# Kernel tuning notes

Hardware: AMD Instinct MI355X
Metric: run time of the kernel (lower is better)

## Reference

```python
import jax, jax.numpy as jnp
import numpy as np

B, C, H, W = 8, 128, 64, 64
GROUPS = 8
EPS = 1e-5


def setup_inputs() -> dict:
    key = jax.random.key(0)
    ks = jax.random.split(key, 4)
    x = jax.random.normal(ks[0], (B, C, H, W), dtype=jnp.float32)
    gamma = jnp.ones((C,), jnp.float32)
    beta = jnp.zeros((C,), jnp.float32)
    w_qkv = jax.random.normal(ks[1], (3 * C, C), jnp.float32) * (C ** -0.5)
    b_qkv = jnp.zeros((3 * C,), jnp.float32)
    w_proj = jax.random.normal(ks[2], (C, C), jnp.float32) * (C ** -0.5)
    b_proj = jnp.zeros((C,), jnp.float32)
    return {"x": x, "gamma": gamma, "beta": beta, "w_qkv": w_qkv,
            "b_qkv": b_qkv, "w_proj": w_proj, "b_proj": b_proj}


def group_norm(x, gamma, beta):
    b, c, h, w = x.shape
    xg = x.reshape(b, GROUPS, c // GROUPS, h, w)
    mean = xg.mean(axis=(2, 3, 4), keepdims=True)
    var = xg.var(axis=(2, 3, 4), keepdims=True)
    xn = ((xg - mean) * jax.lax.rsqrt(var + EPS)).reshape(b, c, h, w)
    return xn * gamma[None, :, None, None] + beta[None, :, None, None]


def reference(x, gamma, beta, w_qkv, b_qkv, w_proj, b_proj):
    b, c, h, w = x.shape
    n = h * w
    hn = group_norm(x, gamma, beta)
    # 1x1 conv == channel matmul
    qkv = jnp.einsum('oc,bchw->bohw', w_qkv, hn) + b_qkv[None, :, None, None]
    q, k, v = jnp.split(qkv.reshape(b, 3 * c, n), 3, axis=1)  # each [b,c,n]
    attn = jax.nn.softmax(jnp.einsum('bci,bcj->bij', q, k) * (c ** -0.5), axis=-1)
    out = jnp.einsum('bij,bcj->bci', attn, v).reshape(b, c, h, w)
    proj = jnp.einsum('oc,bchw->bohw', w_proj, out) + b_proj[None, :, None, None]
    return x + proj
```

## Files before the change

kernel.cpp:

```cpp
#include <hip/hip_runtime.h>
#include <cstdint>

#define NB 8
#define NC 128
#define NPIX 4096
#define NGROUP 8
#define CPG 16
#define EPS_GN 1e-5f
#define QSCALE 0.12751879523604132f
#define NSPLIT 2
#define JTILES (NPIX / 64 / NSPLIT)

typedef __attribute__((ext_vector_type(8))) short short8;
typedef __attribute__((ext_vector_type(16))) float f32x16;
typedef __attribute__((ext_vector_type(2))) int int2v;

typedef __attribute__((address_space(1))) const void gvoid_t;
typedef __attribute__((address_space(3))) void svoid_t;

__device__ __forceinline__ unsigned packbf(float lo, float hi) {
  unsigned r;
  asm("v_cvt_pk_bf16_f32 %0, %1, %2" : "=v"(r) : "v"(lo), "v"(hi));
  return r;
}
__device__ __forceinline__ ushort bf16of(float v) {
  return (ushort)(packbf(v, v) & 0xffffu);
}
__device__ __forceinline__ float bfl(unsigned w) {
  return __builtin_bit_cast(float, w << 16);
}
__device__ __forceinline__ float bfh(unsigned w) {
  return __builtin_bit_cast(float, w & 0xffff0000u);
}

__device__ __forceinline__ void plswap(unsigned& a, unsigned& b) {
  int2v r = __builtin_amdgcn_permlane32_swap((int)a, (int)b, false, false);
  a = (unsigned)r[0];
  b = (unsigned)r[1];
}

__device__ __forceinline__ int swK(int row) {
  return ((row & 7) << 1) | ((row >> 3) & 1);
}

__global__ __launch_bounds__(256) void k_pre(const float* __restrict__ x,
                                             float* __restrict__ stats,
                                             const float* __restrict__ wqkv,
                                             const float* __restrict__ wproj,
                                             ushort* __restrict__ wbuf) {
  int blk = blockIdx.x;
  if (blk < 64) {
    const float4* base = (const float4*)(x + (size_t)blk * CPG * NPIX);
    float s = 0.f, ss = 0.f;
    for (int i = threadIdx.x; i < CPG * NPIX / 4; i += 256) {
      float4 v = base[i];
      s  += v.x + v.y + v.z + v.w;
      ss += v.x * v.x + v.y * v.y + v.z * v.z + v.w * v.w;
    }
#pragma unroll
    for (int off = 32; off >= 1; off >>= 1) {
      s  += __shfl_down(s, off);
      ss += __shfl_down(ss, off);
    }
    __shared__ float red[8];
    int wid = threadIdx.x >> 6;
    if ((threadIdx.x & 63) == 0) { red[wid] = s; red[4 + wid] = ss; }
    __syncthreads();
    if (threadIdx.x == 0) {
      float S  = red[0] + red[1] + red[2] + red[3];
      float SS = red[4] + red[5] + red[6] + red[7];
      float mean = S * (1.f / (CPG * NPIX));
      float var  = SS * (1.f / (CPG * NPIX)) - mean * mean;
      stats[blk * 2]     = mean;
      stats[blk * 2 + 1] = rsqrtf(var + EPS_GN);
    }
  } else {
    int gi = (blk - 64) * 256 + threadIdx.x;
    int t = gi >> 11, ci = gi & 2047;
    int o = ci >> 4, cc = (ci & 15) ^ (o & 7);
    const float* src = (t < 3) ? (wqkv + ((size_t)(t * 128 + o) * 128 + cc * 8))
                               : (wproj + ((size_t)o * 128 + cc * 8));
    float4 a = *(const float4*)src;
    float4 b2 = *(const float4*)(src + 4);
    uint4 pk;
    pk.x = packbf(a.x, a.y);  pk.y = packbf(a.z, a.w);
    pk.z = packbf(b2.x, b2.y); pk.w = packbf(b2.z, b2.w);
    *(uint4*)&wbuf[(size_t)gi << 3] = pk;
  }
}

__global__ __launch_bounds__(256) void k_qkv(const float* __restrict__ x,
                                             const float* __restrict__ stats,
                                             const float* __restrict__ gamma,
                                             const float* __restrict__ beta,
                                             const ushort* __restrict__ wbuf,
                                             const float* __restrict__ bias,
                                             ushort* __restrict__ qT,
                                             ushort* __restrict__ kT,
                                             ushort* __restrict__ vB) {
  __shared__ ushort At[128 * 128];
  __shared__ ushort Bt[128 * 128];
  __shared__ float sArr[128], tArr[128], biasS[384];
  int b = blockIdx.x, pt = blockIdx.y;
  int p0 = pt * 128;
  int tid = threadIdx.x;
  if (tid < 128) {
    int g = tid >> 4;
    float mean = stats[(b * NGROUP + g) * 2];
    float rstd = stats[(b * NGROUP + g) * 2 + 1];
    float sc = rstd * gamma[tid];
    sArr[tid] = sc;
    tArr[tid] = beta[tid] - mean * sc;
  }
  for (int i = tid; i < 384; i += 256) biasS[i] = bias[i];
  __syncthreads();
  const float* xb = x + (size_t)b * NC * NPIX;
#pragma unroll
  for (int u = 0; u < 8; ++u) {
    int task = tid + u * 256;
    int p = task & 127, cc = task >> 7;
    int c0 = cc * 8;
    float v[8];
#pragma unroll
    for (int i = 0; i < 8; ++i)
      v[i] = sArr[c0 + i] * xb[(size_t)(c0 + i) * NPIX + p0 + p] + tArr[c0 + i];
    uint4 pk;
    pk.x = packbf(v[0], v[1]); pk.y = packbf(v[2], v[3]);
    pk.z = packbf(v[4], v[5]); pk.w = packbf(v[6], v[7]);
    *(uint4*)&Bt[((p << 4) + (cc ^ (p & 7))) << 3] = pk;
  }
  int lane = tid & 63, wv = tid >> 6;
  int lq = lane & 31, h = lane >> 5;

  for (int ot = 0; ot < 3; ++ot) {
    __syncthreads();
#pragma unroll
    for (int u = 0; u < 8; ++u) {
      int g = u * 4 + wv;
      __builtin_amdgcn_global_load_lds(
          (gvoid_t*)(wbuf + (((size_t)ot * 2048 + g * 64 + lane) << 3)),
          (svoid_t*)(At + (g << 9)), 16, 0, 0);
    }
    __syncthreads();
    short8 af[8];
    int arow = wv * 32 + lq;
#pragma unroll
    for (int kk = 0; kk < 8; ++kk) {
      int ch = kk * 2 + h;
      af[kk] = *(const short8*)&At[((arow << 4) + (ch ^ (arow & 7))) << 3];
    }
#pragma unroll
    for (int np = 0; np < 2; ++np) {
      int nt0 = np * 2, nt1 = np * 2 + 1;
      int br0 = nt0 * 32 + lq, br1 = nt1 * 32 + lq;
      f32x16 a0, a1;
#pragma unroll
      for (int r = 0; r < 16; ++r) { a0[r] = 0.f; a1[r] = 0.f; }
      __builtin_amdgcn_s_setprio(1);
#pragma unroll
      for (int kk = 0; kk < 8; ++kk) {
        int ch = kk * 2 + h;
        short8 h0 = *(const short8*)&Bt[((br0 << 4) + (ch ^ (br0 & 7))) << 3];
        short8 h1 = *(const short8*)&Bt[((br1 << 4) + (ch ^ (br1 & 7))) << 3];
        a0 = __builtin_amdgcn_mfma_f32_32x32x16_bf16(af[kk], h0, a0, 0, 0, 0);
        a1 = __builtin_amdgcn_mfma_f32_32x32x16_bf16(af[kk], h1, a1, 0, 0, 0);
      }
      __builtin_amdgcn_s_setprio(0);
#pragma unroll
      for (int half = 0; half < 2; ++half) {
        f32x16& acc = half ? a1 : a0;
        int pg = p0 + (half ? nt1 : nt0) * 32 + lq;
        if (ot < 2) {
          ushort* dst = (ot == 0) ? qT : kT;
          float sc = (ot == 0) ? QSCALE : 1.0f;
#pragma unroll
          for (int g2 = 0; g2 < 4; ++g2) {
            int orow = wv * 32 + 4 * h + 8 * g2;
            uint2 st;
            st.x = packbf((acc[g2 * 4 + 0] + biasS[ot * 128 + orow + 0]) * sc,
                          (acc[g2 * 4 + 1] + biasS[ot * 128 + orow + 1]) * sc);
            st.y = packbf((acc[g2 * 4 + 2] + biasS[ot * 128 + orow + 2]) * sc,
                          (acc[g2 * 4 + 3] + biasS[ot * 128 + orow + 3]) * sc);
            *(uint2*)&dst[(((size_t)b << 12) + pg) * 128 + orow] = st;
          }
        } else {
#pragma unroll
          for (int r = 0; r < 16; ++r) {
            int orow = wv * 32 + (r & 3) + 8 * (r >> 2) + 4 * h;
            float vv = acc[r] + biasS[256 + orow];
            vB[((size_t)(b * 128 + orow) << 12) + pg] = bf16of(vv);
          }
        }
      }
    }
  }
}

__device__ __forceinline__ void attn_tile(const ushort* __restrict__ cur,
                                          const short8 (&qf)[8],
                                          f32x16 (&pacc)[4],
                                          float& m_run, float& l_run,
                                          int lq, int h, int swk) {
  f32x16 s0, s1;
#pragma unroll
  for (int r = 0; r < 16; ++r) { s0[r] = 0.f; s1[r] = 0.f; }
  __builtin_amdgcn_s_setprio(1);
#pragma unroll
  for (int kk = 0; kk < 8; ++kk) {
    int ch = (kk << 1) + h;
    short8 kf0 = *(const short8*)&cur[(((lq) << 4) + (ch ^ swk)) << 3];
    short8 kf1 = *(const short8*)&cur[(((32 + lq) << 4) + (ch ^ swk)) << 3];
    s0 = __builtin_amdgcn_mfma_f32_32x32x16_bf16(kf0, qf[kk], s0, 0, 0, 0);
    s1 = __builtin_amdgcn_mfma_f32_32x32x16_bf16(kf1, qf[kk], s1, 0, 0, 0);
  }
  __builtin_amdgcn_s_setprio(0);

  float tm[8];
#pragma unroll
  for (int r = 0; r < 8; ++r)
    tm[r] = fmaxf(fmaxf(s0[2 * r], s0[2 * r + 1]), fmaxf(s1[2 * r], s1[2 * r + 1]));
  float tmax = fmaxf(fmaxf(fmaxf(tm[0], tm[1]), fmaxf(tm[2], tm[3])),
                     fmaxf(fmaxf(tm[4], tm[5]), fmaxf(tm[6], tm[7])));
  tmax = fmaxf(tmax, __shfl_xor(tmax, 32));

  bool noresc = __all(tmax - m_run <= 8.f);
  float mcur = noresc ? m_run : fmaxf(m_run, tmax);

#pragma unroll
  for (int r = 0; r < 16; ++r) { s0[r] = exp2f(s0[r] - mcur); }
#pragma unroll
  for (int r = 0; r < 16; ++r) { s1[r] = exp2f(s1[r] - mcur); }

  float alpha = 1.f;
  if (!noresc) {
    alpha = exp2f(m_run - mcur);
    m_run = mcur;
#pragma unroll
    for (int r = 0; r < 16; ++r) {
      int qr = (r & 3) + ((r >> 2) << 3) + (h << 2);
      float av = __shfl(alpha, qr);
      pacc[0][r] *= av; pacc[1][r] *= av; pacc[2][r] *= av; pacc[3][r] *= av;
    }
  }

  short8 pa[4];
#pragma unroll
  for (int kk = 0; kk < 4; ++kk) {
    float v0, v1, v2, v3, v4, v5, v6, v7;
    if (kk == 0)      { v0=s0[0];v1=s0[1];v2=s0[2];v3=s0[3];v4=s0[4];v5=s0[5];v6=s0[6];v7=s0[7]; }
    else if (kk == 1) { v0=s0[8];v1=s0[9];v2=s0[10];v3=s0[11];v4=s0[12];v5=s0[13];v6=s0[14];v7=s0[15]; }
    else if (kk == 2) { v0=s1[0];v1=s1[1];v2=s1[2];v3=s1[3];v4=s1[4];v5=s1[5];v6=s1[6];v7=s1[7]; }
    else              { v0=s1[8];v1=s1[9];v2=s1[10];v3=s1[11];v4=s1[12];v5=s1[13];v6=s1[14];v7=s1[15]; }
    unsigned P0a = packbf(v0, v1), P0b = packbf(v2, v3);
    unsigned P1a = packbf(v4, v5), P1b = packbf(v6, v7);
    plswap(P0a, P1a);
    plswap(P0b, P1b);
    uint4 wv;
    wv.x = P0a;  wv.y = P0b;
    wv.z = P1a;  wv.w = P1b;
    pa[kk] = __builtin_bit_cast(short8, wv);
  }

  __builtin_amdgcn_s_setprio(1);
#pragma unroll
  for (int nt = 0; nt < 4; ++nt) {
    int row = (nt << 5) + lq;
#pragma unroll
    for (int kk = 0; kk < 4; ++kk) {
      int ch = (kk << 1) + h;
      short8 vf = *(const short8*)&cur[8192 + (((row << 3) + (ch ^ (lq & 7))) << 3)];
      pacc[nt] = __builtin_amdgcn_mfma_f32_32x32x16_bf16(pa[kk], vf, pacc[nt], 0, 0, 0);
    }
  }
  __builtin_amdgcn_s_setprio(0);

  float a0 = (s0[0] + s0[1]) + (s0[2] + s0[3]);
  float a1 = (s0[4] + s0[5]) + (s0[6] + s0[7]);
  float a2 = (s0[8] + s0[9]) + (s0[10] + s0[11]);
  float a3 = (s0[12] + s0[13]) + (s0[14] + s0[15]);
  float a4 = (s1[0] + s1[1]) + (s1[2] + s1[3]);
  float a5 = (s1[4] + s1[5]) + (s1[6] + s1[7]);
  float a6 = (s1[8] + s1[9]) + (s1[10] + s1[11]);
  float a7 = (s1[12] + s1[13]) + (s1[14] + s1[15]);
  float sum = ((a0 + a1) + (a2 + a3)) + ((a4 + a5) + (a6 + a7));
  sum += __shfl_xor(sum, 32);
  l_run = noresc ? (l_run + sum) : (l_run * alpha + sum);
}

__global__ __launch_bounds__(256, 2) void k_attn(const ushort* __restrict__ qT,
                                                 const ushort* __restrict__ kT,
                                                 const ushort* __restrict__ vB,
                                                 ushort* __restrict__ attP,
                                                 float2* __restrict__ mlv) {
  __shared__ ushort lds[32768];
  int tid = threadIdx.x;
  int b = blockIdx.x, qt = blockIdx.y, s = blockIdx.z;
  int wid = tid >> 6;
  int lane = tid & 63;
  int lq = lane & 31;
  int h = lane >> 5;
  int swk = swK(lq);
  int q0 = qt * 128 + wid * 32;
  int jbase = s * (NPIX / NSPLIT);

  short8 qf[8];
  const ushort* qp = qT + (((size_t)b << 12) + q0 + lq) * 128 + h * 8;
#pragma unroll
  for (int kk = 0; kk < 8; ++kk) qf[kk] = *(const short8*)(qp + kk * 16);

  f32x16 pacc[4];
#pragma unroll
  for (int nt = 0; nt < 4; ++nt)
#pragma unroll
    for (int r = 0; r < 16; ++r) pacc[nt][r] = 0.f;
  float m_run = -1e30f, l_run = 0.f;

  int id0 = wid * 64 + lane;
  int krow0 = id0 >> 4, kch0 = id0 & 15;
  int vrow0 = id0 >> 3, vch0 = id0 & 7;
  const ushort* kbase = kT + (((size_t)b << 12) + jbase + krow0) * 128 +
                        ((kch0 ^ swK(krow0)) << 3);
  const ushort* vbase = vB + ((size_t)(b * 128 + vrow0) << 12) + jbase +
                        ((vch0 ^ (vrow0 & 7)) << 3);
  int tstage = 0;

#define STAGE(SEL)                                                              \
  do {                                                                          \
    if (tstage < JTILES) {                                                      \
      ushort* dbase = lds + (SEL) * 16384;                                      \
      _Pragma("unroll") for (int u = 0; u < 4; ++u) {                           \
        __builtin_amdgcn_global_load_lds((gvoid_t*)(kbase + u * 2048),          \
            (svoid_t*)(dbase + (u * 4 + wid) * 512), 16, 0, 0);                 \
        __builtin_amdgcn_global_load_lds((gvoid_t*)(vbase + u * 131072),        \
            (svoid_t*)(dbase + 8192 + (u * 4 + wid) * 512), 16, 0, 0);          \
      }                                                                         \
      kbase += 8192;                                       \
      vbase += 64;                                                 \
      ++tstage;                                                                 \
    }                                                                           \
  } while (0)

  STAGE(0);
  for (int it = 0; it < JTILES / 2; ++it) {
    __syncthreads();
    STAGE(1);
    attn_tile(lds, qf, pacc, m_run, l_run, lq, h, swk);
    __syncthreads();
    STAGE(0);
    attn_tile(lds + 16384, qf, pacc, m_run, l_run, lq, h, swk);
  }
#undef STAGE

  size_t sb = (size_t)(s * NB + b);
#pragma unroll
  for (int r = 0; r < 16; ++r) {
    int qr = (r & 3) + ((r >> 2) << 3) + (h << 2);
    size_t rowbase = (((sb << 12) + q0 + qr) << 7) + lq;
    attP[rowbase]      = bf16of(pacc[0][r]);
    attP[rowbase + 32] = bf16of(pacc[1][r]);
    attP[rowbase + 64] = bf16of(pacc[2][r]);
    attP[rowbase + 96] = bf16of(pacc[3][r]);
  }
  if (h == 0) {
    mlv[(sb << 12) + q0 + lq] = make_float2(m_run, l_run);
  }
}

__global__ __launch_bounds__(256) void k_proj(const float* __restrict__ x,
                                              const ushort* __restrict__ attP,
                                              const float2* __restrict__ mlv,
                                              const ushort* __restrict__ wbuf,
                                              const float* __restrict__ bias,
                                              float* __restrict__ out) {
  __shared__ ushort At[128 * 128];
  __shared__ ushort Bt[128 * 128];
  __shared__ float c0s[128], c1s[128], biasS[128];
  int b = blockIdx.x, pt = blockIdx.y;
  int p0 = pt * 128;
  int tid = threadIdx.x;
  int lane = tid & 63, wv = tid >> 6;
#pragma unroll
  for (int u = 0; u < 8; ++u) {
    int g = u * 4 + wv;
    __builtin_amdgcn_global_load_lds(
        (gvoid_t*)(wbuf + (((size_t)3 * 2048 + g * 64 + lane) << 3)),
        (svoid_t*)(At + (g << 9)), 16, 0, 0);
  }
  if (tid < 128) {
    float2 ml0 = mlv[(((size_t)b) << 12) + p0 + tid];
    float2 ml1 = mlv[(((size_t)(NB + b)) << 12) + p0 + tid];
    float M = fmaxf(ml0.x, ml1.x);
    float e0 = exp2f(ml0.x - M), e1 = exp2f(ml1.x - M);
    float inv = 1.f / (ml0.y * e0 + ml1.y * e1);
    c0s[tid] = e0 * inv;
    c1s[tid] = e1 * inv;
    biasS[tid] = bias[tid];
  }
  __syncthreads();
#pragma unroll
  for (int u = 0; u < 8; ++u) {
    int task = tid + u * 256;
    int p = task & 127, cc = task >> 7;
    const ushort* a0p = attP + ((((size_t)b << 12) + p0 + p) << 7) + cc * 8;
    const ushort* a1p = attP + ((((size_t)(NB + b) << 12) + p0 + p) << 7) + cc * 8;
    uint4 u0 = *(const uint4*)a0p;
    uint4 u1 = *(const uint4*)a1p;
    float c0 = c0s[p], c1 = c1s[p];
    uint4 pk;
    pk.x = packbf(bfl(u0.x) * c0 + bfl(u1.x) * c1,
                  bfh(u0.x) * c0 + bfh(u1.x) * c1);
    pk.y = packbf(bfl(u0.y) * c0 + bfl(u1.y) * c1,
                  bfh(u0.y) * c0 + bfh(u1.y) * c1);
    pk.z = packbf(bfl(u0.z) * c0 + bfl(u1.z) * c1,
                  bfh(u0.z) * c0 + bfh(u1.z) * c1);
    pk.w = packbf(bfl(u0.w) * c0 + bfl(u1.w) * c1,
                  bfh(u0.w) * c0 + bfh(u1.w) * c1);
    *(uint4*)&Bt[((p << 4) + (cc ^ (p & 7))) << 3] = pk;
  }
  __syncthreads();
  int lq = lane & 31, h = lane >> 5;
  short8 af[8];
  int arow = wv * 32 + lq;
#pragma unroll
  for (int kk = 0; kk < 8; ++kk) {
    int ch = kk * 2 + h;
    af[kk] = *(const short8*)&At[((arow << 4) + (ch ^ (arow & 7))) << 3];
  }
  const float* xb = x + (size_t)b * NC * NPIX;
  float* ob = out + (size_t)b * NC * NPIX;
#pragma unroll
  for (int np = 0; np < 2; ++np) {
    int nt0 = np * 2, nt1 = np * 2 + 1;
    int br0 = nt0 * 32 + lq, br1 = nt1 * 32 + lq;
    f32x16 a0, a1;
#pragma unroll
    for (int r = 0; r < 16; ++r) { a0[r] = 0.f; a1[r] = 0.f; }
    __builtin_amdgcn_s_setprio(1);
#pragma unroll
    for (int kk = 0; kk < 8; ++kk) {
      int ch = kk * 2 + h;
      short8 h0 = *(const short8*)&Bt[((br0 << 4) + (ch ^ (br0 & 7))) << 3];
      short8 h1 = *(const short8*)&Bt[((br1 << 4) + (ch ^ (br1 & 7))) << 3];
      a0 = __builtin_amdgcn_mfma_f32_32x32x16_bf16(af[kk], h0, a0, 0, 0, 0);
      a1 = __builtin_amdgcn_mfma_f32_32x32x16_bf16(af[kk], h1, a1, 0, 0, 0);
    }
    __builtin_amdgcn_s_setprio(0);
#pragma unroll
    for (int half = 0; half < 2; ++half) {
      f32x16& acc = half ? a1 : a0;
      int pg = p0 + (half ? nt1 : nt0) * 32 + lq;
#pragma unroll
      for (int r = 0; r < 16; ++r) {
        int orow = wv * 32 + (r & 3) + 8 * (r >> 2) + 4 * h;
        size_t idx = ((size_t)orow << 12) + pg;
        ob[idx] = acc[r] + biasS[orow] + xb[idx];
      }
    }
  }
}

extern "C" void kernel_launch(void* const* d_in, const int* in_sizes, int n_in,
                              void* d_out, int out_size, void* d_ws, size_t ws_size,
                              hipStream_t stream) {
  const float* x      = (const float*)d_in[0];
  const float* gamma  = (const float*)d_in[1];
  const float* beta   = (const float*)d_in[2];
  const float* w_qkv  = (const float*)d_in[3];
  const float* b_qkv  = (const float*)d_in[4];
  const float* w_proj = (const float*)d_in[5];
  const float* b_proj = (const float*)d_in[6];
  float* out = (float*)d_out;
  char* wsb = (char*)d_ws;

  float*  stats = (float*)wsb;
  ushort* qT    = (ushort*)(wsb + 1024);
  ushort* kT    = (ushort*)(wsb + 1024 + (8u << 20));
  ushort* vB    = (ushort*)(wsb + 1024 + (16u << 20));
  ushort* attP  = (ushort*)(wsb + 1024 + (24u << 20));
  float2* mlv   = (float2*)(wsb + 1024 + (40u << 20));
  ushort* wbuf  = (ushort*)(wsb + 1024 + (41u << 20));

  hipLaunchKernelGGL(k_pre, dim3(96), dim3(256), 0, stream,
                     x, stats, w_qkv, w_proj, wbuf);
  hipLaunchKernelGGL(k_qkv, dim3(NB, NPIX / 128), dim3(256), 0, stream,
                     x, stats, gamma, beta, wbuf, b_qkv, qT, kT, vB);
  hipLaunchKernelGGL(k_attn, dim3(NB, NPIX / 128, NSPLIT), dim3(256), 0, stream,
                     qT, kT, vB, attP, mlv);
  hipLaunchKernelGGL(k_proj, dim3(NB, NPIX / 128), dim3(256), 0, stream,
                     x, attP, mlv, wbuf, b_proj, out);
}
```

Baseline: 134.4 us.

## Deepen K/V prefetch with partial vmcnt waits instead of full syncthreads

```diff
diff --git a/kernel.cpp b/kernel.cpp
--- a/kernel.cpp
+++ b/kernel.cpp
@@ -318,36 +318,36 @@
   int id0 = wid * 64 + lane;
   int krow0 = id0 >> 4, kch0 = id0 & 15;
   int vrow0 = id0 >> 3, vch0 = id0 & 7;
-  const ushort* kbase = kT + (((size_t)b << 12) + jbase + krow0) * 128 +
-                        ((kch0 ^ swK(krow0)) << 3);
-  const ushort* vbase = vB + ((size_t)(b * 128 + vrow0) << 12) + jbase +
-                        ((vch0 ^ (vrow0 & 7)) << 3);
-  int tstage = 0;
-
-#define STAGE(SEL)                                                              \
+  const ushort* kInv = kT + (((size_t)b << 12) + jbase + krow0) * 128 +
+                       ((kch0 ^ swK(krow0)) << 3);
+  const ushort* vInv = vB + ((size_t)(b * 128 + vrow0) << 12) + jbase +
+                       ((vch0 ^ (vrow0 & 7)) << 3);
+
+#define STAGE(SEL, JW)                                                          \
   do {                                                                          \
-    if (tstage < JTILES) {                                                      \
-      ushort* dbase = lds + (SEL) * 16384;                                      \
-      _Pragma("unroll") for (int u = 0; u < 4; ++u) {                           \
-        __builtin_amdgcn_global_load_lds((gvoid_t*)(kbase + u * 2048),          \
-            (svoid_t*)(dbase + (u * 4 + wid) * 512), 16, 0, 0);                 \
-        __builtin_amdgcn_global_load_lds((gvoid_t*)(vbase + u * 131072),        \
-            (svoid_t*)(dbase + 8192 + (u * 4 + wid) * 512), 16, 0, 0);          \
-      }                                                                         \
-      kbase += 8192;                                       \
-      vbase += 64;                                                 \
-      ++tstage;                                                                 \
+    ushort* dbase = lds + (SEL) * 16384;                                        \
+    const ushort* ksrc = kInv + (size_t)(JW) * 8192;                            \
+    const ushort* vsrc = vInv + (size_t)(JW) * 64;                              \
+    _Pragma("unroll") for (int u = 0; u < 4; ++u) {                             \
+      __builtin_amdgcn_global_load_lds((gvoid_t*)(ksrc + u * 2048),             \
+          (svoid_t*)(dbase + (u * 4 + wid) * 512), 16, 0, 0);                   \
+      __builtin_amdgcn_global_load_lds((gvoid_t*)(vsrc + u * 131072),           \
+          (svoid_t*)(dbase + 8192 + (u * 4 + wid) * 512), 16, 0, 0);            \
     }                                                                           \
   } while (0)
 
-  STAGE(0);
-  for (int it = 0; it < JTILES / 2; ++it) {
-    __syncthreads();
-    STAGE(1);
-    attn_tile(lds, qf, pacc, m_run, l_run, lq, h, swk);
-    __syncthreads();
-    STAGE(0);
-    attn_tile(lds + 16384, qf, pacc, m_run, l_run, lq, h, swk);
+  STAGE(0, 0);
+  STAGE(1, 1);
+
+  for (int t = 0; t < JTILES; ++t) {
+    asm volatile("s_waitcnt vmcnt(8)" ::: "memory");
+    __builtin_amdgcn_s_barrier();
+    const ushort* cur = lds + (t & 1) * 16384;
+    attn_tile(cur, qf, pacc, m_run, l_run, lq, h, swk);
+    __builtin_amdgcn_s_barrier();
+    int tn = t + 2;
+    if (tn >= JTILES) tn -= JTILES;
+    STAGE(t & 1, tn);
   }
 #undef STAGE
 
```

Result: slower. 141.0 us (+5.0%).
